# Kernel tuning notes

Hardware: AMD Instinct MI355X
Metric: run time of the kernel (lower is better)

The kernel has to match this reference:

```python
import jax, jax.numpy as jnp
import numpy as np

N = 100000      # nodes
E = 600000      # edges per etype
IN = 128        # in_feats
H = 128         # h_feats
NT = 3          # number of edge types


def setup_inputs() -> dict:
    key = jax.random.key(0)
    ks = jax.random.split(key, 20)
    inp = {"feat": jax.random.normal(ks[0], (N, IN), jnp.float32)}
    for i in range(NT):
        inp[f"src{i}"] = jax.random.randint(ks[1 + 2 * i], (E,), 0, N, dtype=jnp.int32)
        inp[f"dst{i}"] = jax.random.randint(ks[2 + 2 * i], (E,), 0, N, dtype=jnp.int32)
    def glorot(k, s):
        return jax.random.normal(k, s, jnp.float32) * np.float32(1.0 / np.sqrt(s[0]))
    for i in range(NT):
        inp[f"We{i}"] = glorot(ks[7 + i], (IN, H))
        inp[f"be{i}"] = jnp.zeros((H,), jnp.float32)
    inp["Wr1"] = glorot(ks[10], (H, H))
    inp["br1"] = jnp.zeros((H,), jnp.float32)
    inp["Wr2"] = glorot(ks[11], (H, IN))
    inp["br2"] = jnp.zeros((IN,), jnp.float32)
    return inp


def graph_conv(feat, src, dst, W, b):
    # DGL GraphConv, norm='both', activation=relu, allow_zero_in_degree=True
    ones = jnp.ones(src.shape[0], feat.dtype)
    out_deg = jnp.maximum(jax.ops.segment_sum(ones, src, num_segments=N), 1.0)
    in_deg = jnp.maximum(jax.ops.segment_sum(ones, dst, num_segments=N), 1.0)
    x = feat * jax.lax.rsqrt(out_deg)[:, None]          # [N, IN] scaled by src norm
    agg = jax.ops.segment_sum(x[src], dst, num_segments=N)  # gather + scatter-add SpMM
    agg = agg * jax.lax.rsqrt(in_deg)[:, None]          # dst norm
    return jax.nn.relu(agg @ W + b)                     # [N, H]


def reference(feat, src0, dst0, src1, dst1, src2, dst2,
              We0, be0, We1, be1, We2, be2, Wr1, br1, Wr2, br2):
    h0 = graph_conv(feat, src0, dst0, We0, be0)
    h1 = graph_conv(feat, src1, dst1, We1, be1)
    h2 = graph_conv(feat, src2, dst2, We2, be2)
    combined = h0 + h1 + h2                              # sum over etypes
    reconstructed = jax.nn.relu(combined @ Wr1 + br1) @ Wr2 + br2  # [N, IN]
    return (reconstructed, h0, h1, h2)
```

## Files before the change

### kernel.cpp

```cpp
#include <hip/hip_runtime.h>

#define NN 100000
#define EE 600000
#define F  128
#define NF (NN * F)
#define NPAD 100096
#define SLOT_CAP 32
#define NBUCK 391
#define BSHIFT 8
#define BCAP 2048
#define ITEMS 16
#define FEATBLK 12500
#define BINBLK 147
#define PREPBLK 320
#define MMBLK 782

typedef __attribute__((ext_vector_type(8))) short short8;
typedef __attribute__((ext_vector_type(4))) float floatx4;

__device__ inline unsigned short f2bf(float x) {
    union { float f; unsigned u; } v; v.f = x;
    unsigned r = v.u + 0x7FFF + ((v.u >> 16) & 1);
    return (unsigned short)(r >> 16);
}
__device__ inline float bf2f(unsigned short b) {
    union { unsigned u; float f; } v; v.u = ((unsigned)b) << 16;
    return v.f;
}

__device__ inline void gld_lds16(const void* g, void* l) {
    __builtin_amdgcn_global_load_lds(
        (const __attribute__((address_space(1))) void*)g,
        (__attribute__((address_space(3))) void*)l, 16, 0, 0);
}

__global__ __launch_bounds__(256) void prep_bin_kernel(
        const float* __restrict__ feat, unsigned short* __restrict__ fb,
        const int* __restrict__ src0, const int* __restrict__ src1,
        const int* __restrict__ src2, const int* __restrict__ dst0,
        const int* __restrict__ dst1, const int* __restrict__ dst2,
        const float* __restrict__ W0, const float* __restrict__ W1,
        const float* __restrict__ W2, const float* __restrict__ W3,
        const float* __restrict__ W4, unsigned short* __restrict__ Wt,
        int* __restrict__ gcnt_d, int* __restrict__ gcnt_s,
        unsigned* __restrict__ bins_d, int* __restrict__ bins_s) {
    __shared__ int hist_d[NBUCK], hist_s[NBUCK];
    __shared__ int base_d[NBUCK], base_s[NBUCK];
    int bid = blockIdx.x, tid = threadIdx.x;

    if (bid < FEATBLK) {
        int t = bid * 256 + tid;
        float4 v = ((const float4*)feat)[t];
        ushort4 r;
        r.x = f2bf(v.x); r.y = f2bf(v.y); r.z = f2bf(v.z); r.w = f2bf(v.w);
        ((ushort4*)fb)[t] = r;
        return;
    }
    if (bid < FEATBLK + 3 * BINBLK) {
        int b2 = bid - FEATBLK;
        int e = b2 / BINBLK, c = b2 % BINBLK;
        const int* sp = (e == 0) ? src0 : (e == 1) ? src1 : src2;
        const int* dp = (e == 0) ? dst0 : (e == 1) ? dst1 : dst2;
        for (int k = tid; k < NBUCK; k += 256) { hist_d[k] = 0; hist_s[k] = 0; }
        __syncthreads();
        int i0 = c * (256 * ITEMS) + tid;
        int sv[ITEMS], dv[ITEMS], rkd[ITEMS], rks[ITEMS];
#pragma unroll
        for (int j = 0; j < ITEMS; ++j) {
            int i = i0 + j * 256;
            if (i < EE) {
                sv[j] = sp[i]; dv[j] = dp[i];
                rkd[j] = atomicAdd(&hist_d[dv[j] >> BSHIFT], 1);
                rks[j] = atomicAdd(&hist_s[sv[j] >> BSHIFT], 1);
            }
        }
        __syncthreads();
        for (int k = tid; k < NBUCK; k += 256) {
            base_d[k] = atomicAdd(&gcnt_d[e * NBUCK + k], hist_d[k]);
            base_s[k] = atomicAdd(&gcnt_s[e * NBUCK + k], hist_s[k]);
        }
        __syncthreads();
#pragma unroll
        for (int j = 0; j < ITEMS; ++j) {
            int i = i0 + j * 256;
            if (i < EE) {
                int bd = dv[j] >> BSHIFT, bs = sv[j] >> BSHIFT;
                int pd = base_d[bd] + rkd[j], ps = base_s[bs] + rks[j];
                if (pd < BCAP)
                    bins_d[(size_t)(e * NBUCK + bd) * BCAP + pd] =
                        ((unsigned)sv[j] << BSHIFT) | ((unsigned)dv[j] & 255u);
                if (ps < BCAP)
                    bins_s[(size_t)(e * NBUCK + bs) * BCAP + ps] = sv[j];
            }
        }
        return;
    }
    int p = bid - FEATBLK - 3 * BINBLK;
    int w = p >> 6;
    const float* W = (w == 0) ? W0 : (w == 1) ? W1 : (w == 2) ? W2 : (w == 3) ? W3 : W4;
    int t = (p & 63) * 256 + tid;
    int k = t >> 7, n = t & 127;
    Wt[w * F * F + n * F + k] = f2bf(W[t]);
}

__global__ __launch_bounds__(256) void mm3_bucket_kernel(
        const unsigned short* __restrict__ Abf,
        const unsigned short* __restrict__ WtBase,
        unsigned short* __restrict__ hpre,
        const int* __restrict__ gcnt_d, const int* __restrict__ gcnt_s,
        const unsigned* __restrict__ bins_d, const int* __restrict__ bins_s,
        int* __restrict__ in_cnt, float* __restrict__ rs,
        int* __restrict__ slots) {
    __shared__ __align__(16) char smem[65536];
    int tid = threadIdx.x;

    if (blockIdx.x < MMBLK) {
        unsigned short* Abuf = (unsigned short*)smem;
        unsigned short* Wbuf = (unsigned short*)(smem + 32768);
        int lane = tid & 63, wv = tid >> 6;
        int row0 = blockIdx.x * F;

        const unsigned short* Asrc = Abf + (size_t)row0 * F;
        for (int i = 0; i < 8; ++i)
            gld_lds16(Asrc + i * 2048 + wv * 512 + lane * 8, Abuf + i * 2048 + wv * 512);
        for (int i = 0; i < 8; ++i)
            gld_lds16(WtBase + i * 2048 + wv * 512 + lane * 8, Wbuf + i * 2048 + wv * 512);
        __syncthreads();

        int wm = (wv >> 1) * 64, wn = (wv & 1) * 64;
        int q = lane >> 4, mr = lane & 15;

        for (int e = 0; e < 3; ++e) {
            floatx4 acc[4][4];
#pragma unroll
            for (int mi = 0; mi < 4; ++mi)
#pragma unroll
                for (int ni = 0; ni < 4; ++ni)
                    acc[mi][ni] = (floatx4){0.f, 0.f, 0.f, 0.f};

#pragma unroll
            for (int k0 = 0; k0 < 128; k0 += 32) {
                short8 af[4], bfv[4];
#pragma unroll
                for (int t2 = 0; t2 < 4; ++t2)
                    af[t2] = *(const short8*)&Abuf[(wm + t2 * 16 + mr) * F + k0 + q * 8];
#pragma unroll
                for (int t2 = 0; t2 < 4; ++t2)
                    bfv[t2] = *(const short8*)&Wbuf[(wn + t2 * 16 + mr) * F + k0 + q * 8];
#pragma unroll
                for (int mi = 0; mi < 4; ++mi)
#pragma unroll
                    for (int ni = 0; ni < 4; ++ni)
                        acc[mi][ni] = __builtin_amdgcn_mfma_f32_16x16x32_bf16(
                            af[mi], bfv[ni], acc[mi][ni], 0, 0, 0);
            }
            __syncthreads();
            if (e < 2) {
                const unsigned short* Wn = WtBase + (size_t)(e + 1) * F * F;
                for (int i = 0; i < 8; ++i)
                    gld_lds16(Wn + i * 2048 + wv * 512 + lane * 8, Wbuf + i * 2048 + wv * 512);
            }

            unsigned short* Cbf = hpre + (size_t)e * NPAD * F;
#pragma unroll
            for (int ni = 0; ni < 4; ++ni) {
                int col = wn + ni * 16 + mr;
#pragma unroll
                for (int mi = 0; mi < 4; ++mi)
#pragma unroll
                    for (int r = 0; r < 4; ++r) {
                        int grow = row0 + wm + mi * 16 + q * 4 + r;
                        Cbf[(size_t)grow * F + col] = f2bf(acc[mi][ni][r]);
                    }
            }
            if (e < 2) __syncthreads();
        }
        return;
    }

    int* cnt  = (int*)smem;
    int* cnt2 = (int*)(smem + 1024);
    int* sl   = (int*)(smem + 2048);
    int b2 = blockIdx.x - MMBLK;
    int e = b2 / NBUCK, b = b2 % NBUCK;
    cnt[tid] = 0; cnt2[tid] = 0;
    __syncthreads();
    int n0 = b << BSHIFT;
    int m = gcnt_d[e * NBUCK + b]; if (m > BCAP) m = BCAP;
    const unsigned* bd = bins_d + (size_t)(e * NBUCK + b) * BCAP;
    for (int k = tid; k < m; k += 256) {
        unsigned v = bd[k];
        int ln = (int)(v & 255u);
        int p = atomicAdd(&cnt[ln], 1);
        if (p < SLOT_CAP) sl[ln * SLOT_CAP + p] = (int)(v >> BSHIFT);
    }
    int m2 = gcnt_s[e * NBUCK + b]; if (m2 > BCAP) m2 = BCAP;
    const int* bs = bins_s + (size_t)(e * NBUCK + b) * BCAP;
    for (int k = tid; k < m2; k += 256) atomicAdd(&cnt2[bs[k] - n0], 1);
    __syncthreads();
    {
        int node = n0 + tid;
        if (node < NN) {
            in_cnt[e * NN + node] = cnt[tid];
            int c = cnt2[tid];
            rs[e * NN + node] = rsqrtf((float)(c < 1 ? 1 : c));
        }
    }
    for (int k = tid; k < 256 * 8; k += 256) {
        int node = n0 + (k >> 3);
        if (node < NN) {
            int4 w = *(const int4*)&sl[(k >> 3) * SLOT_CAP + (k & 7) * 4];
            ((int4*)&slots[((size_t)e * NN + node) * SLOT_CAP])[k & 7] = w;
        }
    }
}

__global__ __launch_bounds__(256) void gather_kernel(
        const unsigned short* __restrict__ hpre,
        const int* __restrict__ slots,
        const int* __restrict__ in_cnt,
        const float* __restrict__ rs,
        const float* __restrict__ be0, const float* __restrict__ be1,
        const float* __restrict__ be2,
        float* __restrict__ h0, float* __restrict__ h1, float* __restrict__ h2,
        unsigned short* __restrict__ hsum) {
    int node = blockIdx.x * 8 + (threadIdx.x >> 5);
    int l = threadIdx.x & 31;
    if (node >= NN) return;

    int cnt3[3];
#pragma unroll
    for (int e = 0; e < 3; ++e) cnt3[e] = in_cnt[e * NN + node];

    float hs[4] = {0.f, 0.f, 0.f, 0.f};
#pragma unroll
    for (int e = 0; e < 3; ++e) {
        int cnt = cnt3[e];
        int lim = cnt < SLOT_CAP ? cnt : SLOT_CAP;
        const int* sl = slots + ((size_t)e * NN + node) * SLOT_CAP;
        const unsigned short* hp = hpre + (size_t)e * NPAD * F;
        const float* rse = rs + (size_t)e * NN;
        float a0[4] = {0.f, 0.f, 0.f, 0.f}, a1[4] = {0.f, 0.f, 0.f, 0.f};
        float a2[4] = {0.f, 0.f, 0.f, 0.f}, a3[4] = {0.f, 0.f, 0.f, 0.f};
        int p = 0;
        for (; p + 4 <= lim; p += 4) {
            int4 s4 = *(const int4*)&sl[p];
            float r0 = rse[s4.x], r1 = rse[s4.y], r2 = rse[s4.z], r3 = rse[s4.w];
            ushort4 v0 = *(const ushort4*)&hp[(size_t)s4.x * F + l * 4];
            ushort4 v1 = *(const ushort4*)&hp[(size_t)s4.y * F + l * 4];
            ushort4 v2 = *(const ushort4*)&hp[(size_t)s4.z * F + l * 4];
            ushort4 v3 = *(const ushort4*)&hp[(size_t)s4.w * F + l * 4];
            a0[0] = fmaf(bf2f(v0.x), r0, a0[0]); a0[1] = fmaf(bf2f(v0.y), r0, a0[1]);
            a0[2] = fmaf(bf2f(v0.z), r0, a0[2]); a0[3] = fmaf(bf2f(v0.w), r0, a0[3]);
            a1[0] = fmaf(bf2f(v1.x), r1, a1[0]); a1[1] = fmaf(bf2f(v1.y), r1, a1[1]);
            a1[2] = fmaf(bf2f(v1.z), r1, a1[2]); a1[3] = fmaf(bf2f(v1.w), r1, a1[3]);
            a2[0] = fmaf(bf2f(v2.x), r2, a2[0]); a2[1] = fmaf(bf2f(v2.y), r2, a2[1]);
            a2[2] = fmaf(bf2f(v2.z), r2, a2[2]); a2[3] = fmaf(bf2f(v2.w), r2, a2[3]);
            a3[0] = fmaf(bf2f(v3.x), r3, a3[0]); a3[1] = fmaf(bf2f(v3.y), r3, a3[1]);
            a3[2] = fmaf(bf2f(v3.z), r3, a3[2]); a3[3] = fmaf(bf2f(v3.w), r3, a3[3]);
        }
        if (p < lim) {
            int4 s4 = *(const int4*)&sl[p];
            int rem = lim - p;
            {
                float r0 = rse[s4.x];
                ushort4 v0 = *(const ushort4*)&hp[(size_t)s4.x * F + l * 4];
                a0[0] = fmaf(bf2f(v0.x), r0, a0[0]); a0[1] = fmaf(bf2f(v0.y), r0, a0[1]);
                a0[2] = fmaf(bf2f(v0.z), r0, a0[2]); a0[3] = fmaf(bf2f(v0.w), r0, a0[3]);
            }
            if (rem >= 2) {
                float r1 = rse[s4.y];
                ushort4 v1 = *(const ushort4*)&hp[(size_t)s4.y * F + l * 4];
                a1[0] = fmaf(bf2f(v1.x), r1, a1[0]); a1[1] = fmaf(bf2f(v1.y), r1, a1[1]);
                a1[2] = fmaf(bf2f(v1.z), r1, a1[2]); a1[3] = fmaf(bf2f(v1.w), r1, a1[3]);
            }
            if (rem >= 3) {
                float r2 = rse[s4.z];
                ushort4 v2 = *(const ushort4*)&hp[(size_t)s4.z * F + l * 4];
                a2[0] = fmaf(bf2f(v2.x), r2, a2[0]); a2[1] = fmaf(bf2f(v2.y), r2, a2[1]);
                a2[2] = fmaf(bf2f(v2.z), r2, a2[2]); a2[3] = fmaf(bf2f(v2.w), r2, a2[3]);
            }
        }
        float rin = rsqrtf((float)(cnt < 1 ? 1 : cnt));
        const float* be = (e == 0) ? be0 : (e == 1) ? be1 : be2;
        float4 bv = *(const float4*)&be[l * 4];
        floatx4 hv;
        hv.x = fmaxf(fmaf((a0[0] + a1[0]) + (a2[0] + a3[0]), rin, bv.x), 0.f);
        hv.y = fmaxf(fmaf((a0[1] + a1[1]) + (a2[1] + a3[1]), rin, bv.y), 0.f);
        hv.z = fmaxf(fmaf((a0[2] + a1[2]) + (a2[2] + a3[2]), rin, bv.z), 0.f);
        hv.w = fmaxf(fmaf((a0[3] + a1[3]) + (a2[3] + a3[3]), rin, bv.w), 0.f);
        float* h = (e == 0) ? h0 : (e == 1) ? h1 : h2;
        __builtin_nontemporal_store(hv, (floatx4*)&h[(size_t)node * F + l * 4]);
        hs[0] += hv.x; hs[1] += hv.y; hs[2] += hv.z; hs[3] += hv.w;
    }
    ushort4 o;
    o.x = f2bf(hs[0]); o.y = f2bf(hs[1]); o.z = f2bf(hs[2]); o.w = f2bf(hs[3]);
    *(ushort4*)&hsum[(size_t)node * F + l * 4] = o;
}

__global__ __launch_bounds__(256) void rec_fused_kernel(
        const unsigned short* __restrict__ Abf,
        const unsigned short* __restrict__ W1t,
        const unsigned short* __restrict__ W2t,
        const float* __restrict__ br1, const float* __restrict__ br2,
        float* __restrict__ rec) {
    __shared__ unsigned short Abuf[F * F];
    __shared__ unsigned short Wbuf[F * F];
    int tid = threadIdx.x;
    int lane = tid & 63, wv = tid >> 6;
    int row0 = blockIdx.x * F;

    for (int i = 0; i < 8; ++i)
        gld_lds16(W1t + i * 2048 + wv * 512 + lane * 8, Wbuf + i * 2048 + wv * 512);
    const unsigned short* Asrc = Abf + (size_t)row0 * F;
    for (int i = 0; i < 8; ++i)
        gld_lds16(Asrc + i * 2048 + wv * 512 + lane * 8, Abuf + i * 2048 + wv * 512);
    __syncthreads();

    int wm = (wv >> 1) * 64, wn = (wv & 1) * 64;
    int q = lane >> 4, mr = lane & 15;

    floatx4 acc[4][4];
#pragma unroll
    for (int mi = 0; mi < 4; ++mi)
#pragma unroll
        for (int ni = 0; ni < 4; ++ni)
            acc[mi][ni] = (floatx4){0.f, 0.f, 0.f, 0.f};

#pragma unroll
    for (int k0 = 0; k0 < 128; k0 += 32) {
        short8 af[4], bfv[4];
#pragma unroll
        for (int t = 0; t < 4; ++t)
            af[t] = *(const short8*)&Abuf[(wm + t * 16 + mr) * F + k0 + q * 8];
#pragma unroll
        for (int t = 0; t < 4; ++t)
            bfv[t] = *(const short8*)&Wbuf[(wn + t * 16 + mr) * F + k0 + q * 8];
#pragma unroll
        for (int mi = 0; mi < 4; ++mi)
#pragma unroll
            for (int ni = 0; ni < 4; ++ni)
                acc[mi][ni] = __builtin_amdgcn_mfma_f32_16x16x32_bf16(
                    af[mi], bfv[ni], acc[mi][ni], 0, 0, 0);
    }

    __syncthreads();
    for (int i = 0; i < 8; ++i)
        gld_lds16(W2t + i * 2048 + wv * 512 + lane * 8, Wbuf + i * 2048 + wv * 512);
#pragma unroll
    for (int ni = 0; ni < 4; ++ni) {
        int col = wn + ni * 16 + mr;
        float bv = br1[col];
#pragma unroll
        for (int mi = 0; mi < 4; ++mi)
#pragma unroll
            for (int r = 0; r < 4; ++r) {
                int lrow = wm + mi * 16 + q * 4 + r;
                Abuf[lrow * F + col] = f2bf(fmaxf(acc[mi][ni][r] + bv, 0.f));
            }
    }
    __syncthreads();

#pragma unroll
    for (int mi = 0; mi < 4; ++mi)
#pragma unroll
        for (int ni = 0; ni < 4; ++ni)
            acc[mi][ni] = (floatx4){0.f, 0.f, 0.f, 0.f};

#pragma unroll
    for (int k0 = 0; k0 < 128; k0 += 32) {
        short8 af[4], bfv[4];
#pragma unroll
        for (int t = 0; t < 4; ++t)
            af[t] = *(const short8*)&Abuf[(wm + t * 16 + mr) * F + k0 + q * 8];
#pragma unroll
        for (int t = 0; t < 4; ++t)
            bfv[t] = *(const short8*)&Wbuf[(wn + t * 16 + mr) * F + k0 + q * 8];
#pragma unroll
        for (int mi = 0; mi < 4; ++mi)
#pragma unroll
            for (int ni = 0; ni < 4; ++ni)
                acc[mi][ni] = __builtin_amdgcn_mfma_f32_16x16x32_bf16(
                    af[mi], bfv[ni], acc[mi][ni], 0, 0, 0);
    }

#pragma unroll
    for (int ni = 0; ni < 4; ++ni) {
        int col = wn + ni * 16 + mr;
        float bv = br2[col];
#pragma unroll
        for (int mi = 0; mi < 4; ++mi)
#pragma unroll
            for (int r = 0; r < 4; ++r) {
                int grow = row0 + wm + mi * 16 + q * 4 + r;
                if (grow < NN)
                    __builtin_nontemporal_store(acc[mi][ni][r] + bv,
                                                &rec[(size_t)grow * F + col]);
            }
    }
}

extern "C" void kernel_launch(void* const* d_in, const int* in_sizes, int n_in,
                              void* d_out, int out_size, void* d_ws, size_t ws_size,
                              hipStream_t stream) {
    const float* feat = (const float*)d_in[0];
    const int* src[3] = {(const int*)d_in[1], (const int*)d_in[3], (const int*)d_in[5]};
    const int* dst[3] = {(const int*)d_in[2], (const int*)d_in[4], (const int*)d_in[6]};
    const float* We[3] = {(const float*)d_in[7], (const float*)d_in[9], (const float*)d_in[11]};
    const float* be[3] = {(const float*)d_in[8], (const float*)d_in[10], (const float*)d_in[12]};
    const float* Wr1 = (const float*)d_in[13];
    const float* br1 = (const float*)d_in[14];
    const float* Wr2 = (const float*)d_in[15];
    const float* br2 = (const float*)d_in[16];

    float* out = (float*)d_out;
    float* rec = out;
    float* h[3] = {out + NF, out + 2 * NF, out + 3 * NF};

    int* gcnt_d = (int*)d_ws;
    int* gcnt_s = gcnt_d + 3 * NBUCK;
    int* in_cnt = gcnt_s + 3 * NBUCK;
    float* rs   = (float*)(in_cnt + 3 * NN);
    unsigned short* Wt     = (unsigned short*)(rs + 3 * NN);
    unsigned short* featbf = Wt + 5 * F * F;
    unsigned short* hsumbf = featbf + (size_t)NPAD * F;
    unsigned short* hpre   = hsumbf + (size_t)NPAD * F;
    int* slots = (int*)(hpre + (size_t)3 * NPAD * F);
    unsigned* bins_d = (unsigned*)(slots + (size_t)3 * NN * SLOT_CAP);
    int*      bins_s = (int*)(bins_d + (size_t)3 * NBUCK * BCAP);

    (void)hipMemsetAsync(gcnt_d, 0, (size_t)6 * NBUCK * sizeof(int), stream);

    prep_bin_kernel<<<FEATBLK + 3 * BINBLK + PREPBLK, 256, 0, stream>>>(
        feat, featbf, src[0], src[1], src[2], dst[0], dst[1], dst[2],
        We[0], We[1], We[2], Wr1, Wr2, Wt, gcnt_d, gcnt_s, bins_d, bins_s);

    mm3_bucket_kernel<<<MMBLK + 3 * NBUCK, 256, 0, stream>>>(
        featbf, Wt, hpre, gcnt_d, gcnt_s, bins_d, bins_s, in_cnt, rs, slots);

    gather_kernel<<<(NN + 7) / 8, 256, 0, stream>>>(
        hpre, slots, in_cnt, rs, be[0], be[1], be[2], h[0], h[1], h[2], hsumbf);

    rec_fused_kernel<<<NPAD / F, 256, 0, stream>>>(
        hsumbf, Wt + 3 * F * F, Wt + 4 * F * F, br1, br2, rec);
}
```

Before: 501.7 us.

## Aggregate raw features before per-etype GEMM and fuse it with reconstruction MLP

Reorders each GraphConv from transform-then-aggregate to aggregate-then-transform. The SpMM gathers the shared fp16 feature rows, then one fused kernel runs the three etype GEMMs with in-degree norm, bias and relu, accumulates the sum, and runs the two reconstruction GEMMs. This drops the separate hpre GEMM pass, its 3x intermediate writes and the hsum round trip, but writes a 3x agg buffer instead. Precision also switches from bf16 to fp16, which gives more mantissa but less range.

```diff
diff --git a/kernel.cpp b/kernel.cpp
--- a/kernel.cpp
+++ b/kernel.cpp
@@ -15,17 +15,15 @@
 #define PREPBLK 320
 #define MMBLK 782
 
-typedef __attribute__((ext_vector_type(8))) short short8;
+typedef __attribute__((ext_vector_type(8))) _Float16 half8;
 typedef __attribute__((ext_vector_type(4))) float floatx4;
-
-__device__ inline unsigned short f2bf(float x) {
-    union { float f; unsigned u; } v; v.f = x;
-    unsigned r = v.u + 0x7FFF + ((v.u >> 16) & 1);
-    return (unsigned short)(r >> 16);
-}
-__device__ inline float bf2f(unsigned short b) {
-    union { unsigned u; float f; } v; v.u = ((unsigned)b) << 16;
-    return v.f;
+typedef __attribute__((ext_vector_type(4))) unsigned short ushortx4;
+
+__device__ inline unsigned short f2h(float x) {
+    union { _Float16 h; unsigned short u; } v; v.h = (_Float16)x; return v.u;
+}
+__device__ inline float h2f(unsigned short u) {
+    union { unsigned short u; _Float16 h; } v; v.u = u; return (float)v.h;
 }
 
 __device__ inline void gld_lds16(const void* g, void* l) {
@@ -51,9 +49,9 @@
     if (bid < FEATBLK) {
         int t = bid * 256 + tid;
         float4 v = ((const float4*)feat)[t];
-        ushort4 r;
-        r.x = f2bf(v.x); r.y = f2bf(v.y); r.z = f2bf(v.z); r.w = f2bf(v.w);
-        ((ushort4*)fb)[t] = r;
+        ushortx4 r;
+        r.x = f2h(v.x); r.y = f2h(v.y); r.z = f2h(v.z); r.w = f2h(v.w);
+        ((ushortx4*)fb)[t] = r;
         return;
     }
     if (bid < FEATBLK + 3 * BINBLK) {
@@ -100,89 +98,17 @@
     const float* W = (w == 0) ? W0 : (w == 1) ? W1 : (w == 2) ? W2 : (w == 3) ? W3 : W4;
     int t = (p & 63) * 256 + tid;
     int k = t >> 7, n = t & 127;
-    Wt[w * F * F + n * F + k] = f2bf(W[t]);
-}
-
-__global__ __launch_bounds__(256) void mm3_bucket_kernel(
-        const unsigned short* __restrict__ Abf,
-        const unsigned short* __restrict__ WtBase,
-        unsigned short* __restrict__ hpre,
+    Wt[w * F * F + n * F + k] = f2h(W[t]);
+}
+
+__global__ __launch_bounds__(256) void bucket_kernel(
         const int* __restrict__ gcnt_d, const int* __restrict__ gcnt_s,
         const unsigned* __restrict__ bins_d, const int* __restrict__ bins_s,
         int* __restrict__ in_cnt, float* __restrict__ rs,
-        int* __restrict__ slots) {
-    __shared__ __align__(16) char smem[65536];
-    int tid = threadIdx.x;
-
-    if (blockIdx.x < MMBLK) {
-        unsigned short* Abuf = (unsigned short*)smem;
-        unsigned short* Wbuf = (unsigned short*)(smem + 32768);
-        int lane = tid & 63, wv = tid >> 6;
-        int row0 = blockIdx.x * F;
-
-        const unsigned short* Asrc = Abf + (size_t)row0 * F;
-        for (int i = 0; i < 8; ++i)
-            gld_lds16(Asrc + i * 2048 + wv * 512 + lane * 8, Abuf + i * 2048 + wv * 512);
-        for (int i = 0; i < 8; ++i)
-            gld_lds16(WtBase + i * 2048 + wv * 512 + lane * 8, Wbuf + i * 2048 + wv * 512);
-        __syncthreads();
-
-        int wm = (wv >> 1) * 64, wn = (wv & 1) * 64;
-        int q = lane >> 4, mr = lane & 15;
-
-        for (int e = 0; e < 3; ++e) {
-            floatx4 acc[4][4];
-#pragma unroll
-            for (int mi = 0; mi < 4; ++mi)
-#pragma unroll
-                for (int ni = 0; ni < 4; ++ni)
-                    acc[mi][ni] = (floatx4){0.f, 0.f, 0.f, 0.f};
-
-#pragma unroll
-            for (int k0 = 0; k0 < 128; k0 += 32) {
-                short8 af[4], bfv[4];
-#pragma unroll
-                for (int t2 = 0; t2 < 4; ++t2)
-                    af[t2] = *(const short8*)&Abuf[(wm + t2 * 16 + mr) * F + k0 + q * 8];
-#pragma unroll
-                for (int t2 = 0; t2 < 4; ++t2)
-                    bfv[t2] = *(const short8*)&Wbuf[(wn + t2 * 16 + mr) * F + k0 + q * 8];
-#pragma unroll
-                for (int mi = 0; mi < 4; ++mi)
-#pragma unroll
-                    for (int ni = 0; ni < 4; ++ni)
-                        acc[mi][ni] = __builtin_amdgcn_mfma_f32_16x16x32_bf16(
-                            af[mi], bfv[ni], acc[mi][ni], 0, 0, 0);
-            }
-            __syncthreads();
-            if (e < 2) {
-                const unsigned short* Wn = WtBase + (size_t)(e + 1) * F * F;
-                for (int i = 0; i < 8; ++i)
-                    gld_lds16(Wn + i * 2048 + wv * 512 + lane * 8, Wbuf + i * 2048 + wv * 512);
-            }
-
-            unsigned short* Cbf = hpre + (size_t)e * NPAD * F;
-#pragma unroll
-            for (int ni = 0; ni < 4; ++ni) {
-                int col = wn + ni * 16 + mr;
-#pragma unroll
-                for (int mi = 0; mi < 4; ++mi)
-#pragma unroll
-                    for (int r = 0; r < 4; ++r) {
-                        int grow = row0 + wm + mi * 16 + q * 4 + r;
-                        Cbf[(size_t)grow * F + col] = f2bf(acc[mi][ni][r]);
-                    }
-            }
-            if (e < 2) __syncthreads();
-        }
-        return;
-    }
-
-    int* cnt  = (int*)smem;
-    int* cnt2 = (int*)(smem + 1024);
-    int* sl   = (int*)(smem + 2048);
-    int b2 = blockIdx.x - MMBLK;
-    int e = b2 / NBUCK, b = b2 % NBUCK;
+        float* __restrict__ rsin, int* __restrict__ slots) {
+    __shared__ int cnt[256], cnt2[256];
+    __shared__ int sl[256 * SLOT_CAP];
+    int e = blockIdx.y, b = blockIdx.x, tid = threadIdx.x;
     cnt[tid] = 0; cnt2[tid] = 0;
     __syncthreads();
     int n0 = b << BSHIFT;
@@ -201,7 +127,9 @@
     {
         int node = n0 + tid;
         if (node < NN) {
-            in_cnt[e * NN + node] = cnt[tid];
+            int ci = cnt[tid];
+            in_cnt[e * NN + node] = ci;
+            rsin[e * NN + node] = rsqrtf((float)(ci < 1 ? 1 : ci));
             int c = cnt2[tid];
             rs[e * NN + node] = rsqrtf((float)(c < 1 ? 1 : c));
         }
@@ -215,30 +143,21 @@
     }
 }
 
-__global__ __launch_bounds__(256) void gather_kernel(
-        const unsigned short* __restrict__ hpre,
+__global__ __launch_bounds__(256) void agg_kernel(
+        const unsigned short* __restrict__ featbf,
         const int* __restrict__ slots,
         const int* __restrict__ in_cnt,
         const float* __restrict__ rs,
-        const float* __restrict__ be0, const float* __restrict__ be1,
-        const float* __restrict__ be2,
-        float* __restrict__ h0, float* __restrict__ h1, float* __restrict__ h2,
-        unsigned short* __restrict__ hsum) {
+        unsigned short* __restrict__ agg) {
     int node = blockIdx.x * 8 + (threadIdx.x >> 5);
     int l = threadIdx.x & 31;
-    if (node >= NN) return;
-
-    int cnt3[3];
-#pragma unroll
-    for (int e = 0; e < 3; ++e) cnt3[e] = in_cnt[e * NN + node];
-
-    float hs[4] = {0.f, 0.f, 0.f, 0.f};
+    if (node >= NPAD) return;
+
 #pragma unroll
     for (int e = 0; e < 3; ++e) {
-        int cnt = cnt3[e];
+        int cnt = (node < NN) ? in_cnt[e * NN + node] : 0;
         int lim = cnt < SLOT_CAP ? cnt : SLOT_CAP;
         const int* sl = slots + ((size_t)e * NN + node) * SLOT_CAP;
-        const unsigned short* hp = hpre + (size_t)e * NPAD * F;
         const float* rse = rs + (size_t)e * NN;
         float a0[4] = {0.f, 0.f, 0.f, 0.f}, a1[4] = {0.f, 0.f, 0.f, 0.f};
         float a2[4] = {0.f, 0.f, 0.f, 0.f}, a3[4] = {0.f, 0.f, 0.f, 0.f};
@@ -246,63 +165,59 @@
         for (; p + 4 <= lim; p += 4) {
             int4 s4 = *(const int4*)&sl[p];
             float r0 = rse[s4.x], r1 = rse[s4.y], r2 = rse[s4.z], r3 = rse[s4.w];
-            ushort4 v0 = *(const ushort4*)&hp[(size_t)s4.x * F + l * 4];
-            ushort4 v1 = *(const ushort4*)&hp[(size_t)s4.y * F + l * 4];
-            ushort4 v2 = *(const ushort4*)&hp[(size_t)s4.z * F + l * 4];
-            ushort4 v3 = *(const ushort4*)&hp[(size_t)s4.w * F + l * 4];
-            a0[0] = fmaf(bf2f(v0.x), r0, a0[0]); a0[1] = fmaf(bf2f(v0.y), r0, a0[1]);
-            a0[2] = fmaf(bf2f(v0.z), r0, a0[2]); a0[3] = fmaf(bf2f(v0.w), r0, a0[3]);
-            a1[0] = fmaf(bf2f(v1.x), r1, a1[0]); a1[1] = fmaf(bf2f(v1.y), r1, a1[1]);
-            a1[2] = fmaf(bf2f(v1.z), r1, a1[2]); a1[3] = fmaf(bf2f(v1.w), r1, a1[3]);
-            a2[0] = fmaf(bf2f(v2.x), r2, a2[0]); a2[1] = fmaf(bf2f(v2.y), r2, a2[1]);
-            a2[2] = fmaf(bf2f(v2.z), r2, a2[2]); a2[3] = fmaf(bf2f(v2.w), r2, a2[3]);
-            a3[0] = fmaf(bf2f(v3.x), r3, a3[0]); a3[1] = fmaf(bf2f(v3.y), r3, a3[1]);
-            a3[2] = fmaf(bf2f(v3.z), r3, a3[2]); a3[3] = fmaf(bf2f(v3.w), r3, a3[3]);
+            ushort4 v0 = *(const ushort4*)&featbf[(size_t)s4.x * F + l * 4];
+            ushort4 v1 = *(const ushort4*)&featbf[(size_t)s4.y * F + l * 4];
+            ushort4 v2 = *(const ushort4*)&featbf[(size_t)s4.z * F + l * 4];
+            ushort4 v3 = *(const ushort4*)&featbf[(size_t)s4.w * F + l * 4];
+            a0[0] = fmaf(h2f(v0.x), r0, a0[0]); a0[1] = fmaf(h2f(v0.y), r0, a0[1]);
+            a0[2] = fmaf(h2f(v0.z), r0, a0[2]); a0[3] = fmaf(h2f(v0.w), r0, a0[3]);
+            a1[0] = fmaf(h2f(v1.x), r1, a1[0]); a1[1] = fmaf(h2f(v1.y), r1, a1[1]);
+            a1[2] = fmaf(h2f(v1.z), r1, a1[2]); a1[3] = fmaf(h2f(v1.w), r1, a1[3]);
+            a2[0] = fmaf(h2f(v2.x), r2, a2[0]); a2[1] = fmaf(h2f(v2.y), r2, a2[1]);
+            a2[2] = fmaf(h2f(v2.z), r2, a2[2]); a2[3] = fmaf(h2f(v2.w), r2, a2[3]);
+            a3[0] = fmaf(h2f(v3.x), r3, a3[0]); a3[1] = fmaf(h2f(v3.y), r3, a3[1]);
+            a3[2] = fmaf(h2f(v3.z), r3, a3[2]); a3[3] = fmaf(h2f(v3.w), r3, a3[3]);
         }
         if (p < lim) {
             int4 s4 = *(const int4*)&sl[p];
             int rem = lim - p;
             {
                 float r0 = rse[s4.x];
-                ushort4 v0 = *(const ushort4*)&hp[(size_t)s4.x * F + l * 4];
-                a0[0] = fmaf(bf2f(v0.x), r0, a0[0]); a0[1] = fmaf(bf2f(v0.y), r0, a0[1]);
-                a0[2] = fmaf(bf2f(v0.z), r0, a0[2]); a0[3] = fmaf(bf2f(v0.w), r0, a0[3]);
+                ushort4 v0 = *(const ushort4*)&featbf[(size_t)s4.x * F + l * 4];
+                a0[0] = fmaf(h2f(v0.x), r0, a0[0]); a0[1] = fmaf(h2f(v0.y), r0, a0[1]);
+                a0[2] = fmaf(h2f(v0.z), r0, a0[2]); a0[3] = fmaf(h2f(v0.w), r0, a0[3]);
             }
             if (rem >= 2) {
                 float r1 = rse[s4.y];
-                ushort4 v1 = *(const ushort4*)&hp[(size_t)s4.y * F + l * 4];
-                a1[0] = fmaf(bf2f(v1.x), r1, a1[0]); a1[1] = fmaf(bf2f(v1.y), r1, a1[1]);
-                a1[2] = fmaf(bf2f(v1.z), r1, a1[2]); a1[3] = fmaf(bf2f(v1.w), r1, a1[3]);
+                ushort4 v1 = *(const ushort4*)&featbf[(size_t)s4.y * F + l * 4];
+                a1[0] = fmaf(h2f(v1.x), r1, a1[0]); a1[1] = fmaf(h2f(v1.y), r1, a1[1]);
+                a1[2] = fmaf(h2f(v1.z), r1, a1[2]); a1[3] = fmaf(h2f(v1.w), r1, a1[3]);
             }
             if (rem >= 3) {
                 float r2 = rse[s4.z];
-                ushort4 v2 = *(const ushort4*)&hp[(size_t)s4.z * F + l * 4];
-                a2[0] = fmaf(bf2f(v2.x), r2, a2[0]); a2[1] = fmaf(bf2f(v2.y), r2, a2[1]);
-                a2[2] = fmaf(bf2f(v2.z), r2, a2[2]); a2[3] = fmaf(bf2f(v2.w), r2, a2[3]);
-            }
-        }
-        float rin = rsqrtf((float)(cnt < 1 ? 1 : cnt));
-        const float* be = (e == 0) ? be0 : (e == 1) ? be1 : be2;
-        float4 bv = *(const float4*)&be[l * 4];
-        floatx4 hv;
-        hv.x = fmaxf(fmaf((a0[0] + a1[0]) + (a2[0] + a3[0]), rin, bv.x), 0.f);
-        hv.y = fmaxf(fmaf((a0[1] + a1[1]) + (a2[1] + a3[1]), rin, bv.y), 0.f);
-        hv.z = fmaxf(fmaf((a0[2] + a1[2]) + (a2[2] + a3[2]), rin, bv.z), 0.f);
-        hv.w = fmaxf(fmaf((a0[3] + a1[3]) + (a2[3] + a3[3]), rin, bv.w), 0.f);
-        float* h = (e == 0) ? h0 : (e == 1) ? h1 : h2;
-        __builtin_nontemporal_store(hv, (floatx4*)&h[(size_t)node * F + l * 4]);
-        hs[0] += hv.x; hs[1] += hv.y; hs[2] += hv.z; hs[3] += hv.w;
-    }
-    ushort4 o;
-    o.x = f2bf(hs[0]); o.y = f2bf(hs[1]); o.z = f2bf(hs[2]); o.w = f2bf(hs[3]);
-    *(ushort4*)&hsum[(size_t)node * F + l * 4] = o;
-}
-
-__global__ __launch_bounds__(256) void rec_fused_kernel(
-        const unsigned short* __restrict__ Abf,
-        const unsigned short* __restrict__ W1t,
-        const unsigned short* __restrict__ W2t,
+                ushort4 v2 = *(const ushort4*)&featbf[(size_t)s4.z * F + l * 4];
+                a2[0] = fmaf(h2f(v2.x), r2, a2[0]); a2[1] = fmaf(h2f(v2.y), r2, a2[1]);
+                a2[2] = fmaf(h2f(v2.z), r2, a2[2]); a2[3] = fmaf(h2f(v2.w), r2, a2[3]);
+            }
+        }
+        ushortx4 o;
+        o.x = f2h((a0[0] + a1[0]) + (a2[0] + a3[0]));
+        o.y = f2h((a0[1] + a1[1]) + (a2[1] + a3[1]));
+        o.z = f2h((a0[2] + a1[2]) + (a2[2] + a3[2]));
+        o.w = f2h((a0[3] + a1[3]) + (a2[3] + a3[3]));
+        __builtin_nontemporal_store(
+            o, (ushortx4*)&agg[((size_t)e * NPAD + node) * F + l * 4]);
+    }
+}
+
+__global__ __launch_bounds__(256) void h_rec_kernel(
+        const unsigned short* __restrict__ agg,
+        const unsigned short* __restrict__ Wt,
+        const float* __restrict__ rsin,
+        const float* __restrict__ be0, const float* __restrict__ be1,
+        const float* __restrict__ be2,
         const float* __restrict__ br1, const float* __restrict__ br2,
+        float* __restrict__ h0, float* __restrict__ h1, float* __restrict__ h2,
         float* __restrict__ rec) {
     __shared__ unsigned short Abuf[F * F];
     __shared__ unsigned short Wbuf[F * F];
@@ -311,42 +226,124 @@
     int row0 = blockIdx.x * F;
 
     for (int i = 0; i < 8; ++i)
-        gld_lds16(W1t + i * 2048 + wv * 512 + lane * 8, Wbuf + i * 2048 + wv * 512);
-    const unsigned short* Asrc = Abf + (size_t)row0 * F;
-    for (int i = 0; i < 8; ++i)
-        gld_lds16(Asrc + i * 2048 + wv * 512 + lane * 8, Abuf + i * 2048 + wv * 512);
+        gld_lds16(Wt + i * 2048 + wv * 512 + lane * 8, Wbuf + i * 2048 + wv * 512);
+    {
+        const unsigned short* Asrc = agg + (size_t)row0 * F;
+        for (int i = 0; i < 8; ++i)
+            gld_lds16(Asrc + i * 2048 + wv * 512 + lane * 8, Abuf + i * 2048 + wv * 512);
+    }
     __syncthreads();
 
     int wm = (wv >> 1) * 64, wn = (wv & 1) * 64;
     int q = lane >> 4, mr = lane & 15;
 
+    float hs[4][4][4];
+#pragma unroll
+    for (int mi = 0; mi < 4; ++mi)
+#pragma unroll
+        for (int ni = 0; ni < 4; ++ni)
+#pragma unroll
+            for (int r = 0; r < 4; ++r) hs[mi][ni][r] = 0.f;
+
     floatx4 acc[4][4];
+    for (int e = 0; e < 3; ++e) {
+#pragma unroll
+        for (int mi = 0; mi < 4; ++mi)
+#pragma unroll
+            for (int ni = 0; ni < 4; ++ni)
+                acc[mi][ni] = (floatx4){0.f, 0.f, 0.f, 0.f};
+#pragma unroll
+        for (int k0 = 0; k0 < 128; k0 += 32) {
+            half8 af[4], bfv[4];
+#pragma unroll
+            for (int t2 = 0; t2 < 4; ++t2)
+                af[t2] = *(const half8*)&Abuf[(wm + t2 * 16 + mr) * F + k0 + q * 8];
+#pragma unroll
+            for (int t2 = 0; t2 < 4; ++t2)
+                bfv[t2] = *(const half8*)&Wbuf[(wn + t2 * 16 + mr) * F + k0 + q * 8];
+#pragma unroll
+            for (int mi = 0; mi < 4; ++mi)
+#pragma unroll
+                for (int ni = 0; ni < 4; ++ni)
+                    acc[mi][ni] = __builtin_amdgcn_mfma_f32_16x16x32_f16(
+                        af[mi], bfv[ni], acc[mi][ni], 0, 0, 0);
+        }
+        __syncthreads();
+        if (e < 2) {
+            const unsigned short* Wn = Wt + (size_t)(e + 1) * F * F;
+            for (int i = 0; i < 8; ++i)
+                gld_lds16(Wn + i * 2048 + wv * 512 + lane * 8, Wbuf + i * 2048 + wv * 512);
+            const unsigned short* An = agg + (size_t)(e + 1) * NPAD * F + (size_t)row0 * F;
+            for (int i = 0; i < 8; ++i)
+                gld_lds16(An + i * 2048 + wv * 512 + lane * 8, Abuf + i * 2048 + wv * 512);
+        } else {
+            const unsigned short* Wn = Wt + (size_t)3 * F * F;
+            for (int i = 0; i < 8; ++i)
+                gld_lds16(Wn + i * 2048 + wv * 512 + lane * 8, Wbuf + i * 2048 + wv * 512);
+        }
+
+        const float* be = (e == 0) ? be0 : (e == 1) ? be1 : be2;
+        float* h = (e == 0) ? h0 : (e == 1) ? h1 : h2;
+        const float* rse = rsin + (size_t)e * NN;
+#pragma unroll
+        for (int ni = 0; ni < 4; ++ni) {
+            int col = wn + ni * 16 + mr;
+            float bev = be[col];
+#pragma unroll
+            for (int mi = 0; mi < 4; ++mi)
+#pragma unroll
+                for (int r = 0; r < 4; ++r) {
+                    int grow = row0 + wm + mi * 16 + q * 4 + r;
+                    float ri = (grow < NN) ? rse[grow] : 0.f;
+                    float v = fmaxf(fmaf(acc[mi][ni][r], ri, bev), 0.f);
+                    if (grow < NN)
+                        __builtin_nontemporal_store(v, &h[(size_t)grow * F + col]);
+                    hs[mi][ni][r] += v;
+                }
+        }
+        __syncthreads();
+    }
+
+#pragma unroll
+    for (int ni = 0; ni < 4; ++ni) {
+        int col = wn + ni * 16 + mr;
+#pragma unroll
+        for (int mi = 0; mi < 4; ++mi)
+#pragma unroll
+            for (int r = 0; r < 4; ++r) {
+                int lrow = wm + mi * 16 + q * 4 + r;
+                Abuf[lrow * F + col] = f2h(hs[mi][ni][r]);
+            }
+    }
+    __syncthreads();
+
 #pragma unroll
     for (int mi = 0; mi < 4; ++mi)
 #pragma unroll
         for (int ni = 0; ni < 4; ++ni)
             acc[mi][ni] = (floatx4){0.f, 0.f, 0.f, 0.f};
-
 #pragma unroll
     for (int k0 = 0; k0 < 128; k0 += 32) {
-        short8 af[4], bfv[4];
-#pragma unroll
-        for (int t = 0; t < 4; ++t)
-            af[t] = *(const short8*)&Abuf[(wm + t * 16 + mr) * F + k0 + q * 8];
-#pragma unroll
-        for (int t = 0; t < 4; ++t)
-            bfv[t] = *(const short8*)&Wbuf[(wn + t * 16 + mr) * F + k0 + q * 8];
+        half8 af[4], bfv[4];
+#pragma unroll
+        for (int t2 = 0; t2 < 4; ++t2)
+            af[t2] = *(const half8*)&Abuf[(wm + t2 * 16 + mr) * F + k0 + q * 8];
+#pragma unroll
+        for (int t2 = 0; t2 < 4; ++t2)
+            bfv[t2] = *(const half8*)&Wbuf[(wn + t2 * 16 + mr) * F + k0 + q * 8];
 #pragma unroll
         for (int mi = 0; mi < 4; ++mi)
 #pragma unroll
             for (int ni = 0; ni < 4; ++ni)
-                acc[mi][ni] = __builtin_amdgcn_mfma_f32_16x16x32_bf16(
+                acc[mi][ni] = __builtin_amdgcn_mfma_f32_16x16x32_f16(
                     af[mi], bfv[ni], acc[mi][ni], 0, 0, 0);
     }
-
-    __syncthreads();
-    for (int i = 0; i < 8; ++i)
-        gld_lds16(W2t + i * 2048 + wv * 512 + lane * 8, Wbuf + i * 2048 + wv * 512);
+    __syncthreads();
+    {
+        const unsigned short* Wn = Wt + (size_t)4 * F * F;
+        for (int i = 0; i < 8; ++i)
+            gld_lds16(Wn + i * 2048 + wv * 512 + lane * 8, Wbuf + i * 2048 + wv * 512);
+    }
 #pragma unroll
     for (int ni = 0; ni < 4; ++ni) {
         int col = wn + ni * 16 + mr;
@@ -356,7 +353,7 @@
 #pragma unroll
             for (int r = 0; r < 4; ++r) {
                 int lrow = wm + mi * 16 + q * 4 + r;
-                Abuf[lrow * F + col] = f2bf(fmaxf(acc[mi][ni][r] + bv, 0.f));
+                Abuf[lrow * F + col] = f2h(fmaxf(acc[mi][ni][r] + bv, 0.f));
             }
     }
     __syncthreads();
@@ -366,24 +363,22 @@
 #pragma unroll
         for (int ni = 0; ni < 4; ++ni)
             acc[mi][ni] = (floatx4){0.f, 0.f, 0.f, 0.f};
-
 #pragma unroll
     for (int k0 = 0; k0 < 128; k0 += 32) {
-        short8 af[4], bfv[4];
-#pragma unroll
-        for (int t = 0; t < 4; ++t)
-            af[t] = *(const short8*)&Abuf[(wm + t * 16 + mr) * F + k0 + q * 8];
-#pragma unroll
-        for (int t = 0; t < 4; ++t)
-            bfv[t] = *(const short8*)&Wbuf[(wn + t * 16 + mr) * F + k0 + q * 8];
+        half8 af[4], bfv[4];
+#pragma unroll
+        for (int t2 = 0; t2 < 4; ++t2)
+            af[t2] = *(const half8*)&Abuf[(wm + t2 * 16 + mr) * F + k0 + q * 8];
+#pragma unroll
+        for (int t2 = 0; t2 < 4; ++t2)
+            bfv[t2] = *(const half8*)&Wbuf[(wn + t2 * 16 + mr) * F + k0 + q * 8];
 #pragma unroll
         for (int mi = 0; mi < 4; ++mi)
 #pragma unroll
             for (int ni = 0; ni < 4; ++ni)
-                acc[mi][ni] = __builtin_amdgcn_mfma_f32_16x16x32_bf16(
+                acc[mi][ni] = __builtin_amdgcn_mfma_f32_16x16x32_f16(
                     af[mi], bfv[ni], acc[mi][ni], 0, 0, 0);
     }
-
 #pragma unroll
     for (int ni = 0; ni < 4; ++ni) {
         int col = wn + ni * 16 + mr;
@@ -421,11 +416,11 @@
     int* gcnt_s = gcnt_d + 3 * NBUCK;
     int* in_cnt = gcnt_s + 3 * NBUCK;
     float* rs   = (float*)(in_cnt + 3 * NN);
-    unsigned short* Wt     = (unsigned short*)(rs + 3 * NN);
+    float* rsin = rs + 3 * NN;
+    unsigned short* Wt     = (unsigned short*)(rsin + 3 * NN);
     unsigned short* featbf = Wt + 5 * F * F;
-    unsigned short* hsumbf = featbf + (size_t)NPAD * F;
-    unsigned short* hpre   = hsumbf + (size_t)NPAD * F;
-    int* slots = (int*)(hpre + (size_t)3 * NPAD * F);
+    unsigned short* agg    = featbf + (size_t)NPAD * F;
+    int* slots = (int*)(agg + (size_t)3 * NPAD * F);
     unsigned* bins_d = (unsigned*)(slots + (size_t)3 * NN * SLOT_CAP);
     int*      bins_s = (int*)(bins_d + (size_t)3 * NBUCK * BCAP);
 
@@ -435,12 +430,11 @@
         feat, featbf, src[0], src[1], src[2], dst[0], dst[1], dst[2],
         We[0], We[1], We[2], Wr1, Wr2, Wt, gcnt_d, gcnt_s, bins_d, bins_s);
 
-    mm3_bucket_kernel<<<MMBLK + 3 * NBUCK, 256, 0, stream>>>(
-        featbf, Wt, hpre, gcnt_d, gcnt_s, bins_d, bins_s, in_cnt, rs, slots);
-
-    gather_kernel<<<(NN + 7) / 8, 256, 0, stream>>>(
-        hpre, slots, in_cnt, rs, be[0], be[1], be[2], h[0], h[1], h[2], hsumbf);
-
-    rec_fused_kernel<<<NPAD / F, 256, 0, stream>>>(
-        hsumbf, Wt + 3 * F * F, Wt + 4 * F * F, br1, br2, rec);
-}
+    bucket_kernel<<<dim3(NBUCK, 3), 256, 0, stream>>>(
+        gcnt_d, gcnt_s, bins_d, bins_s, in_cnt, rs, rsin, slots);
+
+    agg_kernel<<<NPAD / 8, 256, 0, stream>>>(featbf, slots, in_cnt, rs, agg);
+
+    h_rec_kernel<<<MMBLK, 256, 0, stream>>>(
+        agg, Wt, rsin, be[0], be[1], be[2], br1, br2, h[0], h[1], h[2], rec);
+}
```

Result: slower. 621.3 us (+23.8%).
